# Optimization experiments

Measured on AMD Instinct MI355X. Metric: run time of the kernel, lower is better.

## Reference

```python
import jax, jax.numpy as jnp
import numpy as np

N_LORAS = 8   # number of adapters (experts)
RANK = 16     # rank per adapter; rmoe = N_LORAS * RANK = 128
TEMP = 1.0    # self.T


def setup_inputs() -> dict:
    key = jax.random.key(0)
    ks = jax.random.split(key, 7)
    B, S, D_IN, D_OUT = 4, 2048, 4096, 4096
    RMOE = N_LORAS * RANK
    x = jax.random.normal(ks[0], (B, S, D_IN), dtype=jnp.float32)
    base_w = jax.random.normal(ks[1], (D_OUT, D_IN), dtype=jnp.float32) / np.sqrt(D_IN)
    base_b = jax.random.normal(ks[2], (D_OUT,), dtype=jnp.float32) * 0.01
    # nn.init.normal_(lora_A.weight, std=1/r); lora_B zero-init in torch, use small random here
    lora_A = jax.random.normal(ks[3], (RMOE, D_IN), dtype=jnp.float32) / RANK
    lora_B = jax.random.normal(ks[4], (D_OUT, RMOE), dtype=jnp.float32) * 0.02
    router_w = jax.random.normal(ks[5], (N_LORAS, D_IN), dtype=jnp.float32) / np.sqrt(D_IN)
    # scaling[name] = lora_alpha / sqrt(r) per adapter (use_rslora)
    scalings = jnp.full((N_LORAS,), 32.0 / np.sqrt(RANK), dtype=jnp.float32)
    return {"x": x, "base_w": base_w, "base_b": base_b, "lora_A": lora_A,
            "lora_B": lora_B, "router_w": router_w, "scalings": scalings, "top_k": 2}


def reference(x, base_w, base_b, lora_A, lora_B, router_w, scalings, top_k):
    # Base dense layer: y = x W^T + b
    base_out = jnp.einsum('bsd,od->bso', x, base_w) + base_b

    # Router: per-token logits over adapters, top-k, softmax over selected
    logits = jnp.einsum('bsd,ed->bse', x, router_w) / TEMP          # [B,S,E]
    topv, topi = jax.lax.top_k(logits, top_k)                        # [B,S,K]
    gate_k = jax.nn.softmax(topv, axis=-1)                           # [B,S,K]
    # dense per-expert gate: scatter top-k weights back to E slots
    gate_e = jnp.sum(jax.nn.one_hot(topi, N_LORAS, dtype=gate_k.dtype)
                     * gate_k[..., None], axis=-2)                   # [B,S,E]

    # Fused LoRA: h = x A^T over the concatenated rank dim, mask ranks by gate*scaling
    h = jnp.einsum('bsd,rd->bsr', x, lora_A)                         # [B,S,RMOE]
    rank_w = jnp.repeat(gate_e * scalings, RANK, axis=-1)            # [B,S,RMOE]
    lora_out = jnp.einsum('bsr,or->bso', h * rank_w, lora_B)         # [B,S,O]

    return base_out + lora_out
```

## Files before the change

kernel.cpp:

```cpp
#include <hip/hip_runtime.h>
#include <cstdint>

typedef unsigned short u16;
typedef float  f32x4 __attribute__((ext_vector_type(4)));
typedef short  s16x4 __attribute__((ext_vector_type(4)));
typedef short  s16x8 __attribute__((ext_vector_type(8)));

#define D_IN  4096
#define D_OUT 4096
#define RMOE  128
#define KAUG  4224
#define NTOK  8192

__device__ __forceinline__ u16 f2bf(float f) {
    unsigned u = __builtin_bit_cast(unsigned, f);
    unsigned r = u + 0x7fffu + ((u >> 16) & 1u);
    return (u16)(r >> 16);
}

__device__ __forceinline__ void gload16(const void* g, void* l) {
    __builtin_amdgcn_global_load_lds(
        (const __attribute__((address_space(1))) void*)g,
        (__attribute__((address_space(3))) void*)l, 16, 0, 0);
}

__global__ __launch_bounds__(256)
void xconv_router_kernel(const float* __restrict__ x, const float* __restrict__ rw,
                         const float* __restrict__ scal,
                         u16* __restrict__ Xaug, float* __restrict__ gates) {
    int wave = threadIdx.x >> 6, lane = threadIdx.x & 63;
    int t = blockIdx.x * 4 + wave;
    const float4* xp = (const float4*)(x + (long)t * D_IN);
    u16* xa = Xaug + (long)t * KAUG;
    float acc[8];
#pragma unroll
    for (int e = 0; e < 8; ++e) acc[e] = 0.f;
#pragma unroll 4
    for (int i = 0; i < 16; ++i) {
        float4 xv = xp[i * 64 + lane];
        s16x4 o;
        o[0] = (short)f2bf(xv.x); o[1] = (short)f2bf(xv.y);
        o[2] = (short)f2bf(xv.z); o[3] = (short)f2bf(xv.w);
        *(s16x4*)(xa + (i * 64 + lane) * 4) = o;
#pragma unroll
        for (int e = 0; e < 8; ++e) {
            float4 wv = ((const float4*)(rw + (long)e * D_IN))[i * 64 + lane];
            acc[e] += xv.x * wv.x + xv.y * wv.y + xv.z * wv.z + xv.w * wv.w;
        }
    }
#pragma unroll
    for (int e = 0; e < 8; ++e) {
#pragma unroll
        for (int off = 32; off > 0; off >>= 1)
            acc[e] += __shfl_xor(acc[e], off, 64);
    }
    if (lane == 0) {
        int i1 = 0; float v1 = acc[0];
#pragma unroll
        for (int e = 1; e < 8; ++e) if (acc[e] > v1) { v1 = acc[e]; i1 = e; }
        int i2 = -1; float v2 = -3.4e38f;
#pragma unroll
        for (int e = 0; e < 8; ++e) if (e != i1 && acc[e] > v2) { v2 = acc[e]; i2 = e; }
        float g1 = 1.f / (1.f + expf(v2 - v1));
        float g2 = 1.f - g1;
        float* gp = gates + (long)t * 8;
#pragma unroll
        for (int e = 0; e < 8; ++e)
            gp[e] = (e == i1) ? g1 * scal[e] : ((e == i2) ? g2 * scal[e] : 0.f);
    }
}

__global__ __launch_bounds__(256)
void convert_rest_kernel(const float* __restrict__ bw,
                         const float* __restrict__ lA, const float* __restrict__ lB,
                         u16* __restrict__ Waug, u16* __restrict__ A16) {
    const long nw = (long)D_OUT * D_IN / 8;
    const long nb = (long)D_OUT * RMOE / 8;
    long tid = (long)blockIdx.x * 256 + threadIdx.x;
    const float* src; u16* dst;
    if (tid < nw) {
        long e = tid * 8; long row = e >> 12; long col = e & 4095;
        src = bw + e; dst = Waug + row * KAUG + col;
    } else if (tid < nw + nb) {
        long e = (tid - nw) * 8; long row = e >> 7; long col = e & 127;
        src = lB + e; dst = Waug + row * KAUG + D_IN + col;
    } else {
        long e = (tid - nw - nb) * 8;
        src = lA + e; dst = A16 + e;
    }
    float4 a = ((const float4*)src)[0];
    float4 b = ((const float4*)src)[1];
    s16x8 o;
    o[0] = (short)f2bf(a.x); o[1] = (short)f2bf(a.y);
    o[2] = (short)f2bf(a.z); o[3] = (short)f2bf(a.w);
    o[4] = (short)f2bf(b.x); o[5] = (short)f2bf(b.y);
    o[6] = (short)f2bf(b.z); o[7] = (short)f2bf(b.w);
    *(s16x8*)dst = o;
}

__global__ __launch_bounds__(256)
void lora_h_kernel(u16* __restrict__ Xaug, const u16* __restrict__ A16,
                   const float* __restrict__ gates) {
    __shared__ u16 sX[64 * 32];
    __shared__ u16 sW[64 * 32];
    int tid = threadIdx.x, wave = tid >> 6, lane = tid & 63;
    int bm = blockIdx.x >> 1, bn = blockIdx.x & 1;
    long m0 = (long)bm * 64; int n0 = bn * 64;
    int wr = wave >> 1, wc = wave & 1;
    int c = wave * 64 + lane, row = c >> 2, oct = c & 3;
    const u16* gx = Xaug + (m0 + row) * KAUG + oct * 8;
    const u16* gw = A16 + (long)(n0 + row) * D_IN + oct * 8;
    u16* lx = sX + wave * 512;
    u16* lw = sW + wave * 512;
    int cl = lane & 15, kh = lane >> 4;
    int aoff[2], boff[2];
#pragma unroll
    for (int i = 0; i < 2; ++i) {
        aoff[i] = (wr * 32 + i * 16 + cl) * 32 + kh * 8;
        boff[i] = (wc * 32 + i * 16 + cl) * 32 + kh * 8;
    }
    f32x4 acc[2][2];
#pragma unroll
    for (int i = 0; i < 2; ++i)
#pragma unroll
        for (int j = 0; j < 2; ++j) acc[i][j] = (f32x4){0.f, 0.f, 0.f, 0.f};
    for (int kt = 0; kt < 128; ++kt) {
        __syncthreads();
        gload16(gx, lx); gload16(gw, lw);
        gx += 32; gw += 32;
        __syncthreads();
        s16x8 a[2], b[2];
#pragma unroll
        for (int i = 0; i < 2; ++i) {
            a[i] = *(const s16x8*)&sX[aoff[i]];
            b[i] = *(const s16x8*)&sW[boff[i]];
        }
#pragma unroll
        for (int mi = 0; mi < 2; ++mi)
#pragma unroll
            for (int ni = 0; ni < 2; ++ni)
                acc[mi][ni] = __builtin_amdgcn_mfma_f32_16x16x32_bf16(
                    a[mi], b[ni], acc[mi][ni], 0, 0, 0);
    }
#pragma unroll
    for (int ni = 0; ni < 2; ++ni) {
        int col = n0 + wc * 32 + ni * 16 + cl;
        int g = col >> 4;
#pragma unroll
        for (int mi = 0; mi < 2; ++mi) {
#pragma unroll
            for (int r = 0; r < 4; ++r) {
                long tok = m0 + wr * 32 + mi * 16 + kh * 4 + r;
                float v = acc[mi][ni][r] * gates[tok * 8 + g];
                Xaug[tok * KAUG + D_IN + col] = f2bf(v);
            }
        }
    }
}

__global__ __launch_bounds__(512, 2)
void main_gemm(const u16* __restrict__ Xaug, const u16* __restrict__ Waug,
               const float* __restrict__ bias, float* __restrict__ out) {
    __shared__ u16 lds[4 * 16384];
    const int tid = threadIdx.x;
    const int wave = tid >> 6, lane = tid & 63;
    const int cl = lane & 15, kh = lane >> 4;
    const int wr = wave >> 2, wc = wave & 3;

    int bid = blockIdx.x;
    int swz = (bid & 7) * 64 + (bid >> 3);
    long m0 = (long)(swz & 31) * 256;
    long n0 = (long)(swz >> 5) * 256;

    const int rA = tid >> 2;
    const int sl = (((tid & 3) ^ ((tid >> 3) & 3))) * 8;
    const u16* gA0 = Xaug + (m0 + rA) * KAUG + sl;
    const u16* gA1 = Xaug + (m0 + 128 + rA) * KAUG + sl;
    const u16* gB0 = Waug + (n0 + rA) * KAUG + sl;
    const u16* gB1 = Waug + (n0 + 128 + rA) * KAUG + sl;
    const int wbase = wave * 512;

    const int swk = (kh ^ ((cl >> 1) & 3)) * 8;
    const int aob = (wr * 128 + cl) * 32 + swk;
    const int bob = 8192 + (wc * 64 + cl) * 32 + swk;

    f32x4 acc[8][4];
#pragma unroll
    for (int m = 0; m < 8; ++m)
#pragma unroll
        for (int n = 0; n < 4; ++n) acc[m][n] = (f32x4){0.f, 0.f, 0.f, 0.f};

#define STAGE_A(t) do { u16* L = lds + ((t) & 3) * 16384 + wbase;            \
        gload16(gA0 + (t) * 32, L);                                          \
        gload16(gA1 + (t) * 32, L + 4096); } while (0)
#define STAGE_B(t) do { u16* L = lds + ((t) & 3) * 16384 + wbase;            \
        gload16(gB0 + (t) * 32, L + 8192);                                   \
        gload16(gB1 + (t) * 32, L + 12288); } while (0)

    STAGE_A(0); STAGE_B(0); STAGE_A(1); STAGE_B(1); STAGE_A(2); STAGE_B(2);

    for (int t = 0; t < 132; ++t) {
        if (t < 130)        asm volatile("s_waitcnt vmcnt(8)" ::: "memory");
        else if (t == 130)  asm volatile("s_waitcnt vmcnt(4)" ::: "memory");
        else                asm volatile("s_waitcnt vmcnt(0)" ::: "memory");
        __builtin_amdgcn_s_barrier();
        __builtin_amdgcn_sched_barrier(0);

        const u16* Lb = lds + (t & 3) * 16384;
        s16x8 av[8], bv[4];
#pragma unroll
        for (int m = 0; m < 4; ++m) av[m] = *(const s16x8*)&Lb[aob + m * 512];
#pragma unroll
        for (int n = 0; n < 4; ++n) bv[n] = *(const s16x8*)&Lb[bob + n * 512];
        if (t + 3 < 132) { STAGE_A(t + 3); STAGE_B(t + 3); }
#pragma unroll
        for (int m = 4; m < 8; ++m) av[m] = *(const s16x8*)&Lb[aob + m * 512];
        __builtin_amdgcn_sched_barrier(0);
        __builtin_amdgcn_s_setprio(1);
#pragma unroll
        for (int m = 0; m < 4; ++m)
#pragma unroll
            for (int n = 0; n < 4; ++n)
                acc[m][n] = __builtin_amdgcn_mfma_f32_16x16x32_bf16(
                    av[m], bv[n], acc[m][n], 0, 0, 0);
        __builtin_amdgcn_s_setprio(0);
        __builtin_amdgcn_sched_barrier(0);
        __builtin_amdgcn_s_setprio(1);
#pragma unroll
        for (int m = 4; m < 8; ++m)
#pragma unroll
            for (int n = 0; n < 4; ++n)
                acc[m][n] = __builtin_amdgcn_mfma_f32_16x16x32_bf16(
                    av[m], bv[n], acc[m][n], 0, 0, 0);
        __builtin_amdgcn_s_setprio(0);
    }
#undef STAGE_A
#undef STAGE_B

#pragma unroll
    for (int n = 0; n < 4; ++n) {
        long col = n0 + wc * 64 + n * 16 + cl;
        float bvv = bias[col];
#pragma unroll
        for (int m = 0; m < 8; ++m) {
            long row = m0 + wr * 128 + m * 16 + kh * 4;
#pragma unroll
            for (int r = 0; r < 4; ++r)
                out[(row + r) * (long)D_OUT + col] = acc[m][n][r] + bvv;
        }
    }
}

extern "C" void kernel_launch(void* const* d_in, const int* in_sizes, int n_in,
                              void* d_out, int out_size, void* d_ws, size_t ws_size,
                              hipStream_t stream) {
    const float* x  = (const float*)d_in[0];
    const float* bw = (const float*)d_in[1];
    const float* bb = (const float*)d_in[2];
    const float* lA = (const float*)d_in[3];
    const float* lB = (const float*)d_in[4];
    const float* rw = (const float*)d_in[5];
    const float* sc = (const float*)d_in[6];
    float* out = (float*)d_out;

    char* ws = (char*)d_ws;
    u16* Xaug  = (u16*)ws;
    u16* Waug  = (u16*)(ws + 69206016);
    u16* A16   = (u16*)(ws + 103809024);
    float* gates = (float*)(ws + 104857600);

    xconv_router_kernel<<<2048, 256, 0, stream>>>(x, rw, sc, Xaug, gates);
    convert_rest_kernel<<<8704, 256, 0, stream>>>(bw, lA, lB, Waug, A16);
    lora_h_kernel<<<256, 256, 0, stream>>>(Xaug, A16, gates);
    main_gemm<<<512, 512, 0, stream>>>(Xaug, Waug, bb, out);
}
```

Measured before the change: 403.4 us.

## Double-buffer LDS fragment reads in registers to overlap with MFMA

The K loop is restructured into pairs of tiles with two register sets of A/B fragments. Each tile's fragments are read from LDS while the MFMAs for the previous tile run, and the global-to-LDS staging is merged into one macro issued after the reads. The aim is to hide LDS read latency behind matrix math instead of stalling before each MFMA block. The cost is about 48 more VGPRs per thread and a more fragile hand-placed waitcnt/barrier schedule, which could lower occupancy.

```diff
diff --git a/kernel.cpp b/kernel.cpp
--- a/kernel.cpp
+++ b/kernel.cpp
@@ -190,52 +190,70 @@
 #pragma unroll
         for (int n = 0; n < 4; ++n) acc[m][n] = (f32x4){0.f, 0.f, 0.f, 0.f};
 
-#define STAGE_A(t) do { u16* L = lds + ((t) & 3) * 16384 + wbase;            \
+#define STAGE(t) do { u16* L = lds + ((t) & 3) * 16384 + wbase;              \
         gload16(gA0 + (t) * 32, L);                                          \
-        gload16(gA1 + (t) * 32, L + 4096); } while (0)
-#define STAGE_B(t) do { u16* L = lds + ((t) & 3) * 16384 + wbase;            \
+        gload16(gA1 + (t) * 32, L + 4096);                                   \
         gload16(gB0 + (t) * 32, L + 8192);                                   \
         gload16(gB1 + (t) * 32, L + 12288); } while (0)
-
-    STAGE_A(0); STAGE_B(0); STAGE_A(1); STAGE_B(1); STAGE_A(2); STAGE_B(2);
-
-    for (int t = 0; t < 132; ++t) {
-        if (t < 130)        asm volatile("s_waitcnt vmcnt(8)" ::: "memory");
-        else if (t == 130)  asm volatile("s_waitcnt vmcnt(4)" ::: "memory");
-        else                asm volatile("s_waitcnt vmcnt(0)" ::: "memory");
+#define READL(av, bv, Lb) do {                                               \
+        _Pragma("unroll")                                                    \
+        for (int m_ = 0; m_ < 8; ++m_)                                       \
+            av[m_] = *(const s16x8*)&(Lb)[aob + m_ * 512];                   \
+        _Pragma("unroll")                                                    \
+        for (int n_ = 0; n_ < 4; ++n_)                                       \
+            bv[n_] = *(const s16x8*)&(Lb)[bob + n_ * 512]; } while (0)
+#define DOMFMA(av, bv) do {                                                  \
+        __builtin_amdgcn_s_setprio(1);                                       \
+        _Pragma("unroll")                                                    \
+        for (int m_ = 0; m_ < 8; ++m_)                                       \
+            _Pragma("unroll")                                                \
+            for (int n_ = 0; n_ < 4; ++n_)                                   \
+                acc[m_][n_] = __builtin_amdgcn_mfma_f32_16x16x32_bf16(       \
+                    av[m_], bv[n_], acc[m_][n_], 0, 0, 0);                   \
+        __builtin_amdgcn_s_setprio(0); } while (0)
+
+    s16x8 av0[8], bv0[4], av1[8], bv1[4];
+
+    STAGE(0); STAGE(1); STAGE(2);
+    asm volatile("s_waitcnt vmcnt(8)" ::: "memory");
+    __builtin_amdgcn_s_barrier();
+    __builtin_amdgcn_sched_barrier(0);
+    READL(av0, bv0, (lds + 0));
+
+    for (int u = 0; u < 66; ++u) {
+        const int tA = 2 * u, tB = 2 * u + 1;
+        if (tA <= 128) asm volatile("s_waitcnt vmcnt(4)" ::: "memory");
+        else           asm volatile("s_waitcnt vmcnt(0)" ::: "memory");
         __builtin_amdgcn_s_barrier();
         __builtin_amdgcn_sched_barrier(0);
-
-        const u16* Lb = lds + (t & 3) * 16384;
-        s16x8 av[8], bv[4];
-#pragma unroll
-        for (int m = 0; m < 4; ++m) av[m] = *(const s16x8*)&Lb[aob + m * 512];
-#pragma unroll
-        for (int n = 0; n < 4; ++n) bv[n] = *(const s16x8*)&Lb[bob + n * 512];
-        if (t + 3 < 132) { STAGE_A(t + 3); STAGE_B(t + 3); }
-#pragma unroll
-        for (int m = 4; m < 8; ++m) av[m] = *(const s16x8*)&Lb[aob + m * 512];
+        {
+            const u16* Lb = lds + (tB & 3) * 16384;
+            READL(av1, bv1, Lb);
+            if (tA + 3 < 132) STAGE(tA + 3);
+        }
+        asm volatile("s_waitcnt lgkmcnt(12)" ::: "memory");
         __builtin_amdgcn_sched_barrier(0);
-        __builtin_amdgcn_s_setprio(1);
-#pragma unroll
-        for (int m = 0; m < 4; ++m)
-#pragma unroll
-            for (int n = 0; n < 4; ++n)
-                acc[m][n] = __builtin_amdgcn_mfma_f32_16x16x32_bf16(
-                    av[m], bv[n], acc[m][n], 0, 0, 0);
-        __builtin_amdgcn_s_setprio(0);
-        __builtin_amdgcn_sched_barrier(0);
-        __builtin_amdgcn_s_setprio(1);
-#pragma unroll
-        for (int m = 4; m < 8; ++m)
-#pragma unroll
-            for (int n = 0; n < 4; ++n)
-                acc[m][n] = __builtin_amdgcn_mfma_f32_16x16x32_bf16(
-                    av[m], bv[n], acc[m][n], 0, 0, 0);
-        __builtin_amdgcn_s_setprio(0);
-    }
-#undef STAGE_A
-#undef STAGE_B
+        DOMFMA(av0, bv0);
+        if (tB < 131) {
+            asm volatile("s_waitcnt vmcnt(4)" ::: "memory");
+            __builtin_amdgcn_s_barrier();
+            __builtin_amdgcn_sched_barrier(0);
+            {
+                const u16* Lb = lds + ((tB + 1) & 3) * 16384;
+                READL(av0, bv0, Lb);
+                if (tB + 3 < 132) STAGE(tB + 3);
+            }
+            asm volatile("s_waitcnt lgkmcnt(12)" ::: "memory");
+            __builtin_amdgcn_sched_barrier(0);
+        } else {
+            asm volatile("s_waitcnt lgkmcnt(0)" ::: "memory");
+            __builtin_amdgcn_sched_barrier(0);
+        }
+        DOMFMA(av1, bv1);
+    }
+#undef STAGE
+#undef READL
+#undef DOMFMA
 
 #pragma unroll
     for (int n = 0; n < 4; ++n) {
```

Result: no change. 402.0 us (-0.3%).

## Software-pipeline LDS fragment reads across K-tiles with double-buffered registers

Applied to the files above, without the earlier changes.

Restructures the main GEMM loop so the first half of the next K-tile's fragments (B and low A) are read from LDS while the current tile's high-half MFMAs run. Register fragments are double-buffered and the loop is unrolled by two. Global staging is split into A and B halves with separate barriers and finer vmcnt/lgkmcnt waits. The aim is to hide LDS read latency behind MFMA work, at the cost of more VGPRs and an extra barrier per tile, which could lower occupancy or add a hazard on LDS buffer reuse.

```diff
diff --git a/kernel.cpp b/kernel.cpp
--- a/kernel.cpp
+++ b/kernel.cpp
@@ -196,46 +196,87 @@
 #define STAGE_B(t) do { u16* L = lds + ((t) & 3) * 16384 + wbase;            \
         gload16(gB0 + (t) * 32, L + 8192);                                   \
         gload16(gB1 + (t) * 32, L + 12288); } while (0)
-
-    STAGE_A(0); STAGE_B(0); STAGE_A(1); STAGE_B(1); STAGE_A(2); STAGE_B(2);
-
-    for (int t = 0; t < 132; ++t) {
-        if (t < 130)        asm volatile("s_waitcnt vmcnt(8)" ::: "memory");
-        else if (t == 130)  asm volatile("s_waitcnt vmcnt(4)" ::: "memory");
-        else                asm volatile("s_waitcnt vmcnt(0)" ::: "memory");
-        __builtin_amdgcn_s_barrier();
-        __builtin_amdgcn_sched_barrier(0);
-
-        const u16* Lb = lds + (t & 3) * 16384;
-        s16x8 av[8], bv[4];
-#pragma unroll
-        for (int m = 0; m < 4; ++m) av[m] = *(const s16x8*)&Lb[aob + m * 512];
-#pragma unroll
-        for (int n = 0; n < 4; ++n) bv[n] = *(const s16x8*)&Lb[bob + n * 512];
-        if (t + 3 < 132) { STAGE_A(t + 3); STAGE_B(t + 3); }
-#pragma unroll
-        for (int m = 4; m < 8; ++m) av[m] = *(const s16x8*)&Lb[aob + m * 512];
-        __builtin_amdgcn_sched_barrier(0);
-        __builtin_amdgcn_s_setprio(1);
-#pragma unroll
-        for (int m = 0; m < 4; ++m)
-#pragma unroll
-            for (int n = 0; n < 4; ++n)
-                acc[m][n] = __builtin_amdgcn_mfma_f32_16x16x32_bf16(
-                    av[m], bv[n], acc[m][n], 0, 0, 0);
-        __builtin_amdgcn_s_setprio(0);
-        __builtin_amdgcn_sched_barrier(0);
-        __builtin_amdgcn_s_setprio(1);
-#pragma unroll
-        for (int m = 4; m < 8; ++m)
-#pragma unroll
-            for (int n = 0; n < 4; ++n)
-                acc[m][n] = __builtin_amdgcn_mfma_f32_16x16x32_bf16(
-                    av[m], bv[n], acc[m][n], 0, 0, 0);
-        __builtin_amdgcn_s_setprio(0);
+#define RD_AHI(av, Lb) do {                                                  \
+        av[4] = *(const s16x8*)&(Lb)[aob + 2048];                            \
+        av[5] = *(const s16x8*)&(Lb)[aob + 2560];                            \
+        av[6] = *(const s16x8*)&(Lb)[aob + 3072];                            \
+        av[7] = *(const s16x8*)&(Lb)[aob + 3584]; } while (0)
+#define RD_BALO(av, bv, Lb) do {                                             \
+        bv[0] = *(const s16x8*)&(Lb)[bob];                                   \
+        bv[1] = *(const s16x8*)&(Lb)[bob + 512];                             \
+        bv[2] = *(const s16x8*)&(Lb)[bob + 1024];                            \
+        bv[3] = *(const s16x8*)&(Lb)[bob + 1536];                            \
+        av[0] = *(const s16x8*)&(Lb)[aob];                                   \
+        av[1] = *(const s16x8*)&(Lb)[aob + 512];                             \
+        av[2] = *(const s16x8*)&(Lb)[aob + 1024];                            \
+        av[3] = *(const s16x8*)&(Lb)[aob + 1536]; } while (0)
+#define CL_LO(av, bv) do {                                                   \
+        __builtin_amdgcn_s_setprio(1);                                       \
+        _Pragma("unroll")                                                    \
+        for (int m_ = 0; m_ < 4; ++m_)                                       \
+            _Pragma("unroll")                                                \
+            for (int n_ = 0; n_ < 4; ++n_)                                   \
+                acc[m_][n_] = __builtin_amdgcn_mfma_f32_16x16x32_bf16(       \
+                    av[m_], bv[n_], acc[m_][n_], 0, 0, 0);                   \
+        __builtin_amdgcn_s_setprio(0); } while (0)
+#define CL_HI(av, bv) do {                                                   \
+        __builtin_amdgcn_s_setprio(1);                                       \
+        _Pragma("unroll")                                                    \
+        for (int m_ = 4; m_ < 8; ++m_)                                       \
+            _Pragma("unroll")                                                \
+            for (int n_ = 0; n_ < 4; ++n_)                                   \
+                acc[m_][n_] = __builtin_amdgcn_mfma_f32_16x16x32_bf16(       \
+                    av[m_], bv[n_], acc[m_][n_], 0, 0, 0);                   \
+        __builtin_amdgcn_s_setprio(0); } while (0)
+#define SBAR() __builtin_amdgcn_sched_barrier(0)
+
+#define TILE(t, avC, bvC, avN, bvN) do {                                     \
+                                                                     \
+        asm volatile("s_waitcnt vmcnt(8)" ::: "memory");                     \
+        __builtin_amdgcn_s_barrier();                                        \
+        SBAR();                                                              \
+        if ((t) + 3 < 132) STAGE_A((t) + 3);                                 \
+        { const u16* LbT = lds + ((t) & 3) * 16384; RD_AHI(avC, LbT); }      \
+        asm volatile("s_waitcnt lgkmcnt(4)" ::: "memory");                   \
+        SBAR();                                                              \
+        CL_LO(avC, bvC);                                                     \
+                                                                     \
+        asm volatile("s_waitcnt vmcnt(6)" ::: "memory");                     \
+        __builtin_amdgcn_s_barrier();                                        \
+        SBAR();                                                              \
+        if ((t) + 3 < 132) STAGE_B((t) + 3);                                 \
+        if ((t) < 131) {                                                     \
+            const u16* LbN = lds + (((t) + 1) & 3) * 16384;                  \
+            RD_BALO(avN, bvN, LbN);                                          \
+            asm volatile("s_waitcnt lgkmcnt(8)" ::: "memory");               \
+        } else {                                                             \
+            asm volatile("s_waitcnt lgkmcnt(0)" ::: "memory");               \
+        }                                                                    \
+        SBAR();                                                              \
+        CL_HI(avC, bvC); } while (0)
+
+    s16x8 av0[8], bv0[4], av1[8], bv1[4];
+
+    STAGE_A(0); STAGE_B(0);
+    STAGE_A(1); STAGE_B(1);
+    STAGE_A(2); STAGE_B(2);
+    asm volatile("s_waitcnt vmcnt(8)" ::: "memory");
+    __builtin_amdgcn_s_barrier();
+    SBAR();
+    RD_BALO(av0, bv0, (lds + 0));
+
+    for (int u = 0; u < 66; ++u) {
+        TILE(2 * u,     av0, bv0, av1, bv1);
+        TILE(2 * u + 1, av1, bv1, av0, bv0);
     }
 #undef STAGE_A
 #undef STAGE_B
+#undef RD_AHI
+#undef RD_BALO
+#undef CL_LO
+#undef CL_HI
+#undef SBAR
+#undef TILE
 
 #pragma unroll
     for (int n = 0; n < 4; ++n) {
```

After: 401.1 us. No clear change (-0.6%).
